# Performance work log

Measured on AMD Instinct MI355X. Metric: run time of the kernel, lower is better.

The kernel has to match this reference:

```python
import jax, jax.numpy as jnp
import numpy as np

N = 100000   # input nodes
M = 100000   # output nodes (size = (N, M))
NNZ = 3_200_000  # edges, avg_degree 32
B = 32       # batch
D = 32       # Kaiming channel dim


def setup_inputs() -> dict:
    key = jax.random.key(0)
    k1, k2, k3 = jax.random.split(key, 3)
    # COO indices: row 0 = src (in [0, N)), row 1 = dst (in [0, M))
    indices = jax.random.randint(k1, (2, NNZ), 0, N, dtype=jnp.int32)
    # Kaiming init: randn * sqrt(2/d), as in the torch module when d is given
    values = jax.random.normal(k2, (NNZ,), dtype=jnp.float32) * np.float32((2.0 / D) ** 0.5)
    bias = jnp.zeros((M, 1), dtype=jnp.float32)
    x = jax.random.normal(k3, (B, N, 1), dtype=jnp.float32)
    return {"x": x, "indices": indices, "values": values, "bias": bias}


def reference(x, indices, values, bias):
    # Equivalent of: for each b, sparse.mm(W.T, x[b]) + bias, W in COO (N, M)
    # y[b, m] = sum_{e: dst[e]==m} values[e] * x[b, src[e]] + bias[m]
    src = indices[0]
    dst = indices[1]
    contrib = x[:, src, 0] * values[None, :]           # (B, NNZ) gather-multiply
    y = jax.ops.segment_sum(contrib.T, dst, num_segments=M)  # (M, B) scatter-add
    return (y.T + bias[:, 0][None, :])[..., None]       # (B, M, 1)
```

## Files before the change

### kernel.cpp

```cpp
#include <hip/hip_runtime.h>
#include <hip/hip_fp16.h>
#include <stdint.h>

#define NB 32
#define BIN_SHIFT 5
#define BIN_ROWS 32
#define NBINS_MAX 4096
#define CSHIFT 10
#define NC_MAX 128
#define FPC 32
#define FCHUNK 8192
#define FTHREADS 1024
#define NWAVE (FTHREADS / 64)
#define EPT (FCHUNK / FTHREADS)
#define CAP_C 34816
#define P2CHUNK 8192
#define CH2 ((CAP_C + P2CHUNK - 1) / P2CHUNK)
#define EPT2 (P2CHUNK / FTHREADS)
#define SRC_BITS 18
#define SRC_MASK ((1u << SRC_BITS) - 1)
#define CAP 1408
#define MAXK 6


__global__ void transpose_x_kernel(const float* __restrict__ x,
                                   __half* __restrict__ xt, int N) {
    __shared__ float tile[32][33];
    int n0 = blockIdx.x * 32;
    for (int i = threadIdx.y; i < 32; i += 8) {
        int n = n0 + threadIdx.x;
        tile[i][threadIdx.x] = (n < N) ? x[(size_t)i * N + n] : 0.f;
    }
    __syncthreads();
    for (int i = threadIdx.y; i < 32; i += 8) {
        int n = n0 + i;
        if (n < N) xt[(size_t)n * NB + threadIdx.x] =
            __float2half(tile[threadIdx.x][i]);
    }
}

__global__ void fill_coarse(const int* __restrict__ src,
                            const int* __restrict__ dst,
                            const float* __restrict__ vals,
                            int* __restrict__ cCursor,
                            uint2* __restrict__ cCsr,
                            int* __restrict__ fineCnt,
                            int* __restrict__ ovCount,
                            int* __restrict__ ovList,
                            int nnz, int ncoarse, int nbins) {
    __shared__ int lhist[NC_MAX];
    __shared__ int lbase[NC_MAX];
    __shared__ int fh[NBINS_MAX];
    int t = threadIdx.x;
    int e0 = blockIdx.x * FCHUNK;
    int dcache[EPT];
    for (int i = t; i < NC_MAX; i += FTHREADS) lhist[i] = 0;
    for (int i = t; i < nbins; i += FTHREADS) fh[i] = 0;
    __syncthreads();
#pragma unroll
    for (int q = 0; q < EPT; ++q) {
        int e = e0 + q * FTHREADS + t;
        int d = (e < nnz) ? dst[e] : -1;
        dcache[q] = d;
        if (d >= 0) atomicAdd(&lhist[d >> CSHIFT], 1);
    }
    __syncthreads();
    for (int i = t; i < ncoarse; i += FTHREADS) {
        int c = lhist[i];
        lbase[i] = c ? atomicAdd(&cCursor[i], c) : 0;
        lhist[i] = 0;
    }
    __syncthreads();
#pragma unroll
    for (int q = 0; q < EPT; ++q) {
        int e = e0 + q * FTHREADS + t;
        int d = dcache[q];
        if (d >= 0) {
            int c = d >> CSHIFT;
            int r = lbase[c] + atomicAdd(&lhist[c], 1);
            if (r < CAP_C) {
                uint32_t meta = ((uint32_t)(d & 1023) << SRC_BITS) |
                                (uint32_t)src[e];
                cCsr[(size_t)c * CAP_C + r] =
                    make_uint2(meta, __float_as_uint(vals[e]));
                atomicAdd(&fh[d >> BIN_SHIFT], 1);
            } else {
                int op = atomicAdd(ovCount, 1);
                ovList[op] = e;
            }
        }
    }
    __syncthreads();
    for (int i = t; i < nbins; i += FTHREADS)
        if (fh[i]) atomicAdd(&fineCnt[i], fh[i]);
}

__global__ void fine_scan(const int* __restrict__ fineCnt,
                          int* __restrict__ fineBase,
                          int* __restrict__ fineCursor, int nbins) {
    __shared__ int s[1024];
    int t = threadIdx.x;
    int v[4];
    int sum = 0;
#pragma unroll
    for (int k = 0; k < 4; ++k) {
        int i = t * 4 + k;
        v[k] = (i < nbins) ? fineCnt[i] : 0;
        sum += v[k];
    }
    s[t] = sum;
    __syncthreads();
    for (int off = 1; off < 1024; off <<= 1) {
        int add = (t >= off) ? s[t - off] : 0;
        __syncthreads();
        s[t] += add;
        __syncthreads();
    }
    int run = s[t] - sum;
#pragma unroll
    for (int k = 0; k < 4; ++k) {
        int i = t * 4 + k;
        if (i < nbins) { fineBase[i] = run; fineCursor[i] = run; }
        run += v[k];
    }
}

__global__ void fill_fine(const int* __restrict__ cCursor,
                          const uint2* __restrict__ cCsr,
                          int* __restrict__ fineCursor,
                          uint2* __restrict__ fineCsr) {
    __shared__ int whist[NWAVE][FPC];
    int c = blockIdx.x / CH2;
    int i = blockIdx.x % CH2;
    int n  = min(cCursor[c], CAP_C);
    int j0 = i * P2CHUNK;
    int jn = min(j0 + P2CHUNK, n);
    if (j0 >= jn) return;
    int t = threadIdx.x;
    int w = t >> 6;
    uint2 ecache[EPT2];
    int* wflat = &whist[0][0];
    if (t < NWAVE * FPC) wflat[t] = 0;
    __syncthreads();
    const uint2* reg = cCsr + (size_t)c * CAP_C;
#pragma unroll
    for (int q = 0; q < EPT2; ++q) {
        int j = j0 + q * FTHREADS + t;
        if (j < jn) {
            uint2 e = reg[j];
            ecache[q] = e;
            atomicAdd(&whist[w][(e.x >> 23) & 31], 1);
        }
    }
    __syncthreads();
    if (t < FPC) {
        int total = 0;
#pragma unroll
        for (int w2 = 0; w2 < NWAVE; ++w2) total += whist[w2][t];
        int base = total ? atomicAdd(&fineCursor[c * FPC + t], total) : 0;
        int run = base;
#pragma unroll
        for (int w2 = 0; w2 < NWAVE; ++w2) {
            int cn = whist[w2][t];
            whist[w2][t] = run;
            run += cn;
        }
    }
    __syncthreads();
#pragma unroll
    for (int q = 0; q < EPT2; ++q) {
        int j = j0 + q * FTHREADS + t;
        if (j < jn) {
            uint2 e = ecache[q];
            int p = atomicAdd(&whist[w][(e.x >> 23) & 31], 1);
            fineCsr[p] = e;
        }
    }
}

__global__ __launch_bounds__(256) void sort_gather(
        const int* __restrict__ fineBase,
        const int* __restrict__ fineCursor,
        const uint2* __restrict__ csr,
        const __half* __restrict__ xt,
        const float* __restrict__ bias,
        float* __restrict__ out, int M) {
    __shared__ uint2 sorted[CAP];
    __shared__ int rowCnt[BIN_ROWS];
    __shared__ int rowOff[BIN_ROWS];
    int t = threadIdx.x;
    int bin = blockIdx.x;
    int start = fineBase[bin];
    int cnt   = fineCursor[bin] - start;
    int g = t >> 5;
    int b = t & 31;

    if (cnt <= CAP) {
        uint2 reg[MAXK];
#pragma unroll
        for (int k = 0; k < MAXK; ++k) {
            int j = t + k * 256;
            if (j < cnt) reg[k] = csr[start + j];
        }
        if (t < BIN_ROWS) rowCnt[t] = 0;
        __syncthreads();
#pragma unroll
        for (int k = 0; k < MAXK; ++k) {
            int j = t + k * 256;
            if (j < cnt)
                atomicAdd(&rowCnt[(reg[k].x >> SRC_BITS) & 31], 1);
        }
        __syncthreads();
        if (t == 0) {
            int run = 0;
#pragma unroll
            for (int r = 0; r < BIN_ROWS; ++r) {
                rowOff[r] = run;
                run += rowCnt[r];
            }
        }
        __syncthreads();
#pragma unroll
        for (int k = 0; k < MAXK; ++k) {
            int j = t + k * 256;
            if (j < cnt) {
                int p = atomicAdd(&rowOff[(reg[k].x >> SRC_BITS) & 31], 1);
                sorted[p] = reg[k];
            }
        }
        __syncthreads();
        for (int r = g; r < BIN_ROWS; r += 8) {
            int m = bin * BIN_ROWS + r;
            if (m >= M) break;
            int jend = rowOff[r];
            int jj   = jend - rowCnt[r];
            float acc0 = 0.f, acc1 = 0.f;
            for (; jj + 8 <= jend; jj += 8) {
                uint2 e0 = sorted[jj + 0];
                uint2 e1 = sorted[jj + 1];
                uint2 e2 = sorted[jj + 2];
                uint2 e3 = sorted[jj + 3];
                uint2 e4 = sorted[jj + 4];
                uint2 e5 = sorted[jj + 5];
                uint2 e6 = sorted[jj + 6];
                uint2 e7 = sorted[jj + 7];
                float x0 = __half2float(xt[(size_t)(e0.x & SRC_MASK) * NB + b]);
                float x1 = __half2float(xt[(size_t)(e1.x & SRC_MASK) * NB + b]);
                float x2 = __half2float(xt[(size_t)(e2.x & SRC_MASK) * NB + b]);
                float x3 = __half2float(xt[(size_t)(e3.x & SRC_MASK) * NB + b]);
                float x4 = __half2float(xt[(size_t)(e4.x & SRC_MASK) * NB + b]);
                float x5 = __half2float(xt[(size_t)(e5.x & SRC_MASK) * NB + b]);
                float x6 = __half2float(xt[(size_t)(e6.x & SRC_MASK) * NB + b]);
                float x7 = __half2float(xt[(size_t)(e7.x & SRC_MASK) * NB + b]);
                acc0 = fmaf(__uint_as_float(e0.y), x0, acc0);
                acc1 = fmaf(__uint_as_float(e1.y), x1, acc1);
                acc0 = fmaf(__uint_as_float(e2.y), x2, acc0);
                acc1 = fmaf(__uint_as_float(e3.y), x3, acc1);
                acc0 = fmaf(__uint_as_float(e4.y), x4, acc0);
                acc1 = fmaf(__uint_as_float(e5.y), x5, acc1);
                acc0 = fmaf(__uint_as_float(e6.y), x6, acc0);
                acc1 = fmaf(__uint_as_float(e7.y), x7, acc1);
            }
            for (; jj < jend; ++jj) {
                uint2 e = sorted[jj];
                acc0 = fmaf(__uint_as_float(e.y),
                            __half2float(xt[(size_t)(e.x & SRC_MASK) * NB + b]),
                            acc0);
            }
            out[(size_t)b * M + m] = acc0 + acc1 + bias[m];
        }
    } else {
        float* tile = (float*)sorted;
        for (int i = t; i < BIN_ROWS * NB; i += 256) tile[i] = 0.f;
        __syncthreads();
        for (int j = start + g; j < start + cnt; j += 8) {
            uint2 e = csr[j];
            float xv = __half2float(xt[(size_t)(e.x & SRC_MASK) * NB + b]);
            atomicAdd(&tile[((e.x >> SRC_BITS) & 31) * NB + b],
                      __uint_as_float(e.y) * xv);
        }
        __syncthreads();
        for (int i = t; i < BIN_ROWS * NB; i += 256) {
            int m = bin * BIN_ROWS + (i >> 5);
            if (m < M) out[(size_t)(i & 31) * M + m] = tile[i] + bias[m];
        }
    }
}

__global__ void fixup_kernel(const int* __restrict__ ovCount,
                             const int* __restrict__ ovList,
                             const int* __restrict__ src,
                             const int* __restrict__ dst,
                             const float* __restrict__ vals,
                             const __half* __restrict__ xt,
                             float* __restrict__ out, int M) {
    long long total = (long long)(*ovCount) * 32;
    long long stride = (long long)gridDim.x * blockDim.x;
    for (long long i = (long long)blockIdx.x * blockDim.x + threadIdx.x;
         i < total; i += stride) {
        int k = (int)(i >> 5);
        int b = (int)(i & 31);
        int e = ovList[k];
        atomicAdd(&out[(size_t)b * M + dst[e]],
                  vals[e] * __half2float(xt[(size_t)src[e] * NB + b]));
    }
}

__global__ void finalize_kernel(const float* __restrict__ yt,
                                const float* __restrict__ bias,
                                float* __restrict__ out, int M) {
    __shared__ float tile[32][33];
    int m0 = blockIdx.x * 32;
    for (int i = threadIdx.y; i < 32; i += 8) {
        int m = m0 + i;
        tile[i][threadIdx.x] = (m < M) ? yt[(size_t)m * NB + threadIdx.x] : 0.f;
    }
    __syncthreads();
    for (int i = threadIdx.y; i < 32; i += 8) {
        int m = m0 + threadIdx.x;
        if (m < M) out[(size_t)i * M + m] = tile[threadIdx.x][i] + bias[m];
    }
}

__global__ void scatter_kernel(const int* __restrict__ src,
                               const int* __restrict__ dst,
                               const float* __restrict__ vals,
                               const __half* __restrict__ xt,
                               float* __restrict__ yt, int nnz) {
    long long tid = (long long)blockIdx.x * blockDim.x + threadIdx.x;
    int e = (int)(tid >> 5);
    if (e >= nnz) return;
    int b = (int)(tid & 31);
    atomicAdd(&yt[(size_t)dst[e] * NB + b],
              vals[e] * __half2float(xt[(size_t)src[e] * NB + b]));
}

extern "C" void kernel_launch(void* const* d_in, const int* in_sizes, int n_in,
                              void* d_out, int out_size, void* d_ws, size_t ws_size,
                              hipStream_t stream) {
    const float* x       = (const float*)d_in[0];
    const int*   indices = (const int*)  d_in[1];
    const float* vals    = (const float*)d_in[2];
    const float* bias    = (const float*)d_in[3];

    float* out = (float*)d_out;

    int nnz = in_sizes[1] / 2;
    int N   = in_sizes[0] / NB;
    int M   = in_sizes[3];

    const int* src = indices;
    const int* dst = indices + nnz;

    int nbins   = (M + BIN_ROWS - 1) >> BIN_SHIFT;
    int ncoarse = (M + (1 << CSHIFT) - 1) >> CSHIFT;

    __half* xt         = (__half*)d_ws;
    int*    fineCnt    = (int*)(xt + (size_t)N * NB);
    int*    cCursor    = fineCnt + NBINS_MAX;
    int*    ovCount    = cCursor + NC_MAX;
    int*    fineBase   = ovCount + 4;
    int*    fineCursor = fineBase + NBINS_MAX;
    int*    ovList     = fineCursor + NBINS_MAX;
    uint2*  cCsr       = (uint2*)(((uintptr_t)(ovList + nnz) + 15) &
                                  ~(uintptr_t)15);
    uint2*  fineCsr    = cCsr + (size_t)ncoarse * CAP_C;

    size_t need = (size_t)((char*)(fineCsr + nnz) - (char*)d_ws);

    float* yt = (float*)(xt + (size_t)N * NB);
    size_t need_fb = (size_t)((char*)(yt + (size_t)M * NB) - (char*)d_ws);

    transpose_x_kernel<<<(N + 31) / 32, dim3(32, 8), 0, stream>>>(x, xt, N);

    if (ws_size >= need && nbins <= NBINS_MAX && ncoarse <= NC_MAX) {
        hipMemsetAsync(fineCnt, 0, (NBINS_MAX + NC_MAX + 4) * sizeof(int),
                       stream);
        int fgrid = (nnz + FCHUNK - 1) / FCHUNK;
        fill_coarse<<<fgrid, FTHREADS, 0, stream>>>(src, dst, vals, cCursor,
                                                    cCsr, fineCnt, ovCount,
                                                    ovList, nnz, ncoarse,
                                                    nbins);
        fine_scan<<<1, 1024, 0, stream>>>(fineCnt, fineBase, fineCursor,
                                          nbins);
        fill_fine<<<ncoarse * CH2, FTHREADS, 0, stream>>>(cCursor, cCsr,
                                                          fineCursor, fineCsr);
        sort_gather<<<nbins, 256, 0, stream>>>(fineBase, fineCursor, fineCsr,
                                               xt, bias, out, M);
        fixup_kernel<<<32, 256, 0, stream>>>(ovCount, ovList, src, dst, vals,
                                             xt, out, M);
    } else if (ws_size >= need_fb) {
        hipMemsetAsync(yt, 0, (size_t)M * NB * sizeof(float), stream);
        long long pairs = (long long)nnz * NB;
        int grid = (int)((pairs + 255) / 256);
        scatter_kernel<<<grid, 256, 0, stream>>>(src, dst, vals, xt, yt, nnz);
        finalize_kernel<<<(M + 31) / 32, dim3(32, 8), 0, stream>>>(yt, bias,
                                                                   out, M);
    }
}
```

Baseline: 203.3 us.

## Shrink coarse buckets and compute fine bin offsets locally per bucket

```diff
diff --git a/kernel.cpp b/kernel.cpp
--- a/kernel.cpp
+++ b/kernel.cpp
@@ -6,17 +6,15 @@
 #define BIN_SHIFT 5
 #define BIN_ROWS 32
 #define NBINS_MAX 4096
-#define CSHIFT 10
-#define NC_MAX 128
-#define FPC 32
+#define CSHIFT 8
+#define NC_MAX 512
+#define FPC 8
+#define NWAVE 16
 #define FCHUNK 8192
 #define FTHREADS 1024
-#define NWAVE (FTHREADS / 64)
 #define EPT (FCHUNK / FTHREADS)
-#define CAP_C 34816
-#define P2CHUNK 8192
-#define CH2 ((CAP_C + P2CHUNK - 1) / P2CHUNK)
-#define EPT2 (P2CHUNK / FTHREADS)
+#define CAP_C 9216
+#define EPT2 (CAP_C / FTHREADS)
 #define SRC_BITS 18
 #define SRC_MASK ((1u << SRC_BITS) - 1)
 #define CAP 1408
@@ -44,18 +42,15 @@
                             const float* __restrict__ vals,
                             int* __restrict__ cCursor,
                             uint2* __restrict__ cCsr,
-                            int* __restrict__ fineCnt,
                             int* __restrict__ ovCount,
                             int* __restrict__ ovList,
-                            int nnz, int ncoarse, int nbins) {
+                            int nnz, int ncoarse) {
     __shared__ int lhist[NC_MAX];
     __shared__ int lbase[NC_MAX];
-    __shared__ int fh[NBINS_MAX];
     int t = threadIdx.x;
     int e0 = blockIdx.x * FCHUNK;
     int dcache[EPT];
     for (int i = t; i < NC_MAX; i += FTHREADS) lhist[i] = 0;
-    for (int i = t; i < nbins; i += FTHREADS) fh[i] = 0;
     __syncthreads();
 #pragma unroll
     for (int q = 0; q < EPT; ++q) {
@@ -79,108 +74,78 @@
             int c = d >> CSHIFT;
             int r = lbase[c] + atomicAdd(&lhist[c], 1);
             if (r < CAP_C) {
-                uint32_t meta = ((uint32_t)(d & 1023) << SRC_BITS) |
+                uint32_t meta = ((uint32_t)(d & 255) << SRC_BITS) |
                                 (uint32_t)src[e];
                 cCsr[(size_t)c * CAP_C + r] =
                     make_uint2(meta, __float_as_uint(vals[e]));
-                atomicAdd(&fh[d >> BIN_SHIFT], 1);
             } else {
                 int op = atomicAdd(ovCount, 1);
                 ovList[op] = e;
             }
         }
     }
-    __syncthreads();
-    for (int i = t; i < nbins; i += FTHREADS)
-        if (fh[i]) atomicAdd(&fineCnt[i], fh[i]);
-}
-
-__global__ void fine_scan(const int* __restrict__ fineCnt,
-                          int* __restrict__ fineBase,
-                          int* __restrict__ fineCursor, int nbins) {
-    __shared__ int s[1024];
-    int t = threadIdx.x;
-    int v[4];
-    int sum = 0;
-#pragma unroll
-    for (int k = 0; k < 4; ++k) {
-        int i = t * 4 + k;
-        v[k] = (i < nbins) ? fineCnt[i] : 0;
-        sum += v[k];
-    }
-    s[t] = sum;
-    __syncthreads();
-    for (int off = 1; off < 1024; off <<= 1) {
-        int add = (t >= off) ? s[t - off] : 0;
-        __syncthreads();
-        s[t] += add;
-        __syncthreads();
-    }
-    int run = s[t] - sum;
-#pragma unroll
-    for (int k = 0; k < 4; ++k) {
-        int i = t * 4 + k;
-        if (i < nbins) { fineBase[i] = run; fineCursor[i] = run; }
-        run += v[k];
-    }
-}
-
-__global__ void fill_fine(const int* __restrict__ cCursor,
-                          const uint2* __restrict__ cCsr,
-                          int* __restrict__ fineCursor,
-                          uint2* __restrict__ fineCsr) {
+}
+
+__global__ __launch_bounds__(1024) void fill_fine2(
+        const int* __restrict__ cCursor,
+        const uint2* __restrict__ cCsr,
+        uint2* __restrict__ fineCsr,
+        int* __restrict__ fineBase,
+        int* __restrict__ fineCnt) {
     __shared__ int whist[NWAVE][FPC];
-    int c = blockIdx.x / CH2;
-    int i = blockIdx.x % CH2;
-    int n  = min(cCursor[c], CAP_C);
-    int j0 = i * P2CHUNK;
-    int jn = min(j0 + P2CHUNK, n);
-    if (j0 >= jn) return;
+    __shared__ int fbase[FPC];
+    __shared__ int ftot;
+    int c = blockIdx.x;
+    int n = min(cCursor[c], CAP_C);
     int t = threadIdx.x;
     int w = t >> 6;
-    uint2 ecache[EPT2];
-    int* wflat = &whist[0][0];
-    if (t < NWAVE * FPC) wflat[t] = 0;
+    uint2 ec[EPT2];
+    if (t < NWAVE * FPC) (&whist[0][0])[t] = 0;
     __syncthreads();
     const uint2* reg = cCsr + (size_t)c * CAP_C;
 #pragma unroll
     for (int q = 0; q < EPT2; ++q) {
-        int j = j0 + q * FTHREADS + t;
-        if (j < jn) {
+        int j = q * FTHREADS + t;
+        if (j < n) {
             uint2 e = reg[j];
-            ecache[q] = e;
-            atomicAdd(&whist[w][(e.x >> 23) & 31], 1);
-        }
+            ec[q] = e;
+            atomicAdd(&whist[w][(e.x >> 23) & 7], 1);
+        }
+    }
+    __syncthreads();
+    if (t == 0) {
+        int run = 0;
+        for (int f = 0; f < FPC; ++f) {
+            fbase[f] = run;
+            for (int w2 = 0; w2 < NWAVE; ++w2) {
+                int cn = whist[w2][f];
+                whist[w2][f] = run;
+                run += cn;
+            }
+        }
+        ftot = run;
     }
     __syncthreads();
     if (t < FPC) {
-        int total = 0;
-#pragma unroll
-        for (int w2 = 0; w2 < NWAVE; ++w2) total += whist[w2][t];
-        int base = total ? atomicAdd(&fineCursor[c * FPC + t], total) : 0;
-        int run = base;
-#pragma unroll
-        for (int w2 = 0; w2 < NWAVE; ++w2) {
-            int cn = whist[w2][t];
-            whist[w2][t] = run;
-            run += cn;
-        }
-    }
-    __syncthreads();
+        int gbin = c * FPC + t;
+        fineBase[gbin] = c * CAP_C + fbase[t];
+        int endv = (t == FPC - 1) ? ftot : fbase[t + 1];
+        fineCnt[gbin] = endv - fbase[t];
+    }
 #pragma unroll
     for (int q = 0; q < EPT2; ++q) {
-        int j = j0 + q * FTHREADS + t;
-        if (j < jn) {
-            uint2 e = ecache[q];
-            int p = atomicAdd(&whist[w][(e.x >> 23) & 31], 1);
-            fineCsr[p] = e;
+        int j = q * FTHREADS + t;
+        if (j < n) {
+            uint2 e = ec[q];
+            int p = atomicAdd(&whist[w][(e.x >> 23) & 7], 1);
+            fineCsr[(size_t)c * CAP_C + p] = e;
         }
     }
 }
 
 __global__ __launch_bounds__(256) void sort_gather(
         const int* __restrict__ fineBase,
-        const int* __restrict__ fineCursor,
+        const int* __restrict__ fineCnt,
         const uint2* __restrict__ csr,
         const __half* __restrict__ xt,
         const float* __restrict__ bias,
@@ -191,7 +156,7 @@
     int t = threadIdx.x;
     int bin = blockIdx.x;
     int start = fineBase[bin];
-    int cnt   = fineCursor[bin] - start;
+    int cnt   = fineCnt[bin];
     int g = t >> 5;
     int b = t & 31;
 
@@ -355,18 +320,18 @@
     int nbins   = (M + BIN_ROWS - 1) >> BIN_SHIFT;
     int ncoarse = (M + (1 << CSHIFT) - 1) >> CSHIFT;
 
-    __half* xt         = (__half*)d_ws;
-    int*    fineCnt    = (int*)(xt + (size_t)N * NB);
-    int*    cCursor    = fineCnt + NBINS_MAX;
-    int*    ovCount    = cCursor + NC_MAX;
-    int*    fineBase   = ovCount + 4;
-    int*    fineCursor = fineBase + NBINS_MAX;
-    int*    ovList     = fineCursor + NBINS_MAX;
-    uint2*  cCsr       = (uint2*)(((uintptr_t)(ovList + nnz) + 15) &
-                                  ~(uintptr_t)15);
-    uint2*  fineCsr    = cCsr + (size_t)ncoarse * CAP_C;
-
-    size_t need = (size_t)((char*)(fineCsr + nnz) - (char*)d_ws);
+    __half* xt       = (__half*)d_ws;
+    int*    cCursor  = (int*)(xt + (size_t)N * NB);
+    int*    ovCount  = cCursor + NC_MAX;
+    int*    fineBase = ovCount + 4;
+    int*    fineCnt  = fineBase + NBINS_MAX;
+    int*    ovList   = fineCnt + NBINS_MAX;
+    uint2*  cCsr     = (uint2*)(((uintptr_t)(ovList + nnz) + 15) &
+                                ~(uintptr_t)15);
+    uint2*  fineCsr  = cCsr + (size_t)ncoarse * CAP_C;
+
+    size_t need = (size_t)((char*)(fineCsr + (size_t)ncoarse * CAP_C) -
+                           (char*)d_ws);
 
     float* yt = (float*)(xt + (size_t)N * NB);
     size_t need_fb = (size_t)((char*)(yt + (size_t)M * NB) - (char*)d_ws);
@@ -374,18 +339,14 @@
     transpose_x_kernel<<<(N + 31) / 32, dim3(32, 8), 0, stream>>>(x, xt, N);
 
     if (ws_size >= need && nbins <= NBINS_MAX && ncoarse <= NC_MAX) {
-        hipMemsetAsync(fineCnt, 0, (NBINS_MAX + NC_MAX + 4) * sizeof(int),
-                       stream);
+        hipMemsetAsync(cCursor, 0, (NC_MAX + 4) * sizeof(int), stream);
         int fgrid = (nnz + FCHUNK - 1) / FCHUNK;
         fill_coarse<<<fgrid, FTHREADS, 0, stream>>>(src, dst, vals, cCursor,
-                                                    cCsr, fineCnt, ovCount,
-                                                    ovList, nnz, ncoarse,
-                                                    nbins);
-        fine_scan<<<1, 1024, 0, stream>>>(fineCnt, fineBase, fineCursor,
-                                          nbins);
-        fill_fine<<<ncoarse * CH2, FTHREADS, 0, stream>>>(cCursor, cCsr,
-                                                          fineCursor, fineCsr);
-        sort_gather<<<nbins, 256, 0, stream>>>(fineBase, fineCursor, fineCsr,
+                                                    cCsr, ovCount, ovList,
+                                                    nnz, ncoarse);
+        fill_fine2<<<ncoarse, FTHREADS, 0, stream>>>(cCursor, cCsr, fineCsr,
+                                                     fineBase, fineCnt);
+        sort_gather<<<nbins, 256, 0, stream>>>(fineBase, fineCnt, fineCsr,
                                                xt, bias, out, M);
         fixup_kernel<<<32, 256, 0, stream>>>(ovCount, ovList, src, dst, vals,
                                              xt, out, M);
```

Result: slower. 215.2 us (+5.9%).
